# Performance work log

Hardware: AMD Instinct MI355X
Metric: run time of the kernel (lower is better)

## Reference

```python
import jax, jax.numpy as jnp
import numpy as np

B, T, C = 2, 2048, 1024
N_HEAD = 16
HEAD_DIM = C // N_HEAD

def setup_inputs() -> dict:
    key = jax.random.key(0)
    k1, k2, k3 = jax.random.split(key, 3)
    x = jax.random.normal(k1, (B, T, C), dtype=jnp.float32)
    # Dense kernel init scale ~ 1/sqrt(fan_in) for stable softmax
    w_attn = jax.random.normal(k2, (C, 3 * C), dtype=jnp.float32) / np.sqrt(C)
    w_proj = jax.random.normal(k3, (C, C), dtype=jnp.float32) / np.sqrt(C)
    return {"x": x, "w_attn": w_attn, "w_proj": w_proj}

def reference(x, w_attn, w_proj):
    Bc, Tc, Cc = x.shape
    # QKV projection (use_bias=False)
    qkv = x @ w_attn  # [B, T, 3C]
    q, k, v = jnp.split(qkv, 3, axis=-1)
    # [B, T, C] -> [B, H, T, D]
    def heads(a):
        return a.reshape(Bc, Tc, N_HEAD, HEAD_DIM).swapaxes(1, 2)
    q, k, v = heads(q), heads(k), heads(v)
    scale = 1.0 / jnp.sqrt(jnp.asarray(HEAD_DIM, dtype=x.dtype))
    attn = jnp.einsum('bhqd,bhkd->bhqk', q, k) * scale  # [B, H, T, T]
    attn = jax.nn.softmax(attn, axis=-1)
    # dropout=0.0 / deterministic -> identity
    y = jnp.einsum('bhqk,bhkd->bhqd', attn, v)  # [B, H, T, D]
    y = y.swapaxes(1, 2).reshape(Bc, Tc, Cc)
    return y @ w_proj  # output projection, no bias, dropout identity
```

## Files before the change

### kernel.cpp

```cpp
#include <hip/hip_runtime.h>
#include <hip/hip_bf16.h>

#define B_   2
#define T_   2048
#define C_   1024
#define NH_  16
#define HD_  64

typedef __attribute__((ext_vector_type(8))) short short8;
typedef __attribute__((ext_vector_type(4))) float float4_;
typedef __attribute__((ext_vector_type(4))) _Float16 half4_;
typedef __attribute__((ext_vector_type(2))) __fp16  fp16x2;
typedef __attribute__((ext_vector_type(4))) unsigned short ushort4_;

static __device__ __forceinline__ unsigned short f2bf(float f) {
    union { float f; unsigned u; } v; v.f = f;
    unsigned r = v.u + 0x7fffu + ((v.u >> 16) & 1u);
    return (unsigned short)(r >> 16);
}

static __device__ __forceinline__ void g2l16(const void* g, void* l) {
    __builtin_amdgcn_global_load_lds(
        (const __attribute__((address_space(1))) void*)g,
        (__attribute__((address_space(3))) void*)l, 16, 0, 0);
}

__global__ __launch_bounds__(256) void prep(
    const float* __restrict__ x,      unsigned short* __restrict__ xb,
    const float* __restrict__ wA,     unsigned short* __restrict__ wTa,
    const float* __restrict__ wP,     unsigned short* __restrict__ wTp)
{
    const int t = threadIdx.x;
    int blk = blockIdx.x;
    if (blk < 2048) {
        int i = blk * 256 + t;
        const float4* p = (const float4*)x + (size_t)i * 2;
        float4 a = p[0], b = p[1];
        short8 o;
        o[0]=f2bf(a.x); o[1]=f2bf(a.y); o[2]=f2bf(a.z); o[3]=f2bf(a.w);
        o[4]=f2bf(b.x); o[5]=f2bf(b.y); o[6]=f2bf(b.z); o[7]=f2bf(b.w);
        *((short8*)xb + i) = o;
        return;
    }
    blk -= 2048;
    const float* in; unsigned short* out; int Cc;
    if (blk < 16 * 48) { in = wA; out = wTa; Cc = 3072; }
    else               { blk -= 16 * 48; in = wP; out = wTp; Cc = 1024; }
    const int r0 = (blk % 16) * 64, c0 = (blk / 16) * 64;
    const int R = 1024;
    __shared__ __align__(16) unsigned short Ts[64][72];
    #pragma unroll
    for (int cc = 0; cc < 2; ++cc) {
        int c = cc * 256 + t;
        int r = c >> 3, col = (c & 7) * 8;
        const float* p = in + (size_t)(r0 + r) * Cc + c0 + col;
        #pragma unroll
        for (int i = 0; i < 8; ++i) Ts[col + i][r] = f2bf(p[i]);
    }
    __syncthreads();
    #pragma unroll
    for (int cc = 0; cc < 2; ++cc) {
        int c = cc * 256 + t;
        int cr = c >> 3, oc = (c & 7) * 8;
        uint4 v = *(const uint4*)(&Ts[cr][oc]);
        *(uint4*)(out + (size_t)(c0 + cr) * R + r0 + oc) = v;
    }
}

template <bool C_F32, int BM, bool WRITE_VT>
__global__ __launch_bounds__(256) void gemm_bt(
    const unsigned short* __restrict__ A,
    const unsigned short* __restrict__ Bt,
    void* __restrict__ Cv, unsigned short* __restrict__ vt,
    int M, int N, int K)
{
    __shared__ __align__(16) unsigned short As[BM * 32];
    __shared__ __align__(16) unsigned short Bs[128 * 32];
    const int t = threadIdx.x, lane = t & 63, w = t >> 6;
    const int quad = lane >> 4, ln = lane & 15;
    const int bm = blockIdx.x, bn = blockIdx.y;
    constexpr int NI = (BM == 128) ? 4 : 2;
    const int mw = (BM == 128) ? (w & 1) * 64 : 0;
    const int nw = (BM == 128) ? (w >> 1) * 64 : w * 32;
    float4_ acc[4][NI] = {};

    constexpr int AROWS = BM / 4;
    const unsigned short* Ag = A  + (size_t)(bm * BM + w * AROWS + (lane >> 2)) * K + (lane & 3) * 8;
    const unsigned short* Bg = Bt + (size_t)(bn * 128 + w * 32 + (lane >> 2)) * K + (lane & 3) * 8;
    unsigned short* lA = &As[(w * AROWS) * 32 + lane * 8];
    unsigned short* lB = &Bs[(w * 32) * 32 + lane * 8];

    for (int k0 = 0; k0 < K; k0 += 32) {
        g2l16(Ag + k0, lA);
        if (BM == 128) g2l16(Ag + (size_t)16 * K + k0, lA + 16 * 32);
        g2l16(Bg + k0,                  lB);
        g2l16(Bg + (size_t)16 * K + k0, lB + 16 * 32);
        __syncthreads();
        short8 a[4], b[NI];
        #pragma unroll
        for (int i = 0; i < 4; ++i)
            a[i] = *(const short8*)(&As[(mw + i * 16 + ln) * 32 + quad * 8]);
        #pragma unroll
        for (int i = 0; i < NI; ++i)
            b[i] = *(const short8*)(&Bs[(nw + i * 16 + ln) * 32 + quad * 8]);
        #pragma unroll
        for (int mi = 0; mi < 4; ++mi)
            #pragma unroll
            for (int ni = 0; ni < NI; ++ni)
                acc[mi][ni] = __builtin_amdgcn_mfma_f32_16x16x32_bf16(
                    a[mi], b[ni], acc[mi][ni], 0, 0, 0);
        __syncthreads();
    }

    const int row0 = bm * BM + mw + quad * 4;
    const int col0 = bn * 128 + nw + ln;
    #pragma unroll
    for (int mi = 0; mi < 4; ++mi)
        #pragma unroll
        for (int ni = 0; ni < NI; ++ni) {
            #pragma unroll
            for (int i = 0; i < 4; ++i) {
                size_t idx = (size_t)(row0 + mi * 16 + i) * N + col0 + ni * 16;
                if (C_F32) ((float*)Cv)[idx] = acc[mi][ni][i];
                else       ((unsigned short*)Cv)[idx] = f2bf(acc[mi][ni][i]);
            }
            if (WRITE_VT && col0 + ni * 16 >= 2 * C_) {
                int d     = col0 + ni * 16 - 2 * C_;
                int token = row0 + mi * 16;
                int b     = token >> 11, tloc = token & 2047;
                union { fp16x2 h2[2]; ushort4_ u4; } pk;
                pk.h2[0] = __builtin_amdgcn_cvt_pkrtz(acc[mi][ni][0], acc[mi][ni][1]);
                pk.h2[1] = __builtin_amdgcn_cvt_pkrtz(acc[mi][ni][2], acc[mi][ni][3]);
                *(ushort4_*)(vt + ((size_t)b * 1024 + d) * T_ + tloc) = pk.u4;
            }
        }
}

__device__ __forceinline__ void attn_tile(
    const unsigned short (*Ksb)[72], const unsigned short (*Vsb)[72],
    const short8 (&qf)[2][2], float4_ (&ot)[4][2], float (&ls)[2],
    int quad, int ln)
{
    const float C1 = 0.125f * 1.44269504f;
    const float C2 = 8.0f * 1.44269504f;
    half4_ pf[4][2];
    #pragma unroll
    for (int ct = 0; ct < 4; ++ct) {
        short8 kb0 = *(const short8*)(&Ksb[ct * 16 + ln][quad * 8]);
        short8 kb1 = *(const short8*)(&Ksb[ct * 16 + ln][32 + quad * 8]);
        #pragma unroll
        for (int qm = 0; qm < 2; ++qm) {
            float4_ st = {};
            st = __builtin_amdgcn_mfma_f32_16x16x32_bf16(kb0, qf[qm][0], st, 0, 0, 0);
            st = __builtin_amdgcn_mfma_f32_16x16x32_bf16(kb1, qf[qm][1], st, 0, 0, 0);
            float p0 = __builtin_amdgcn_exp2f(st[0] * C1 - C2);
            float p1 = __builtin_amdgcn_exp2f(st[1] * C1 - C2);
            float p2 = __builtin_amdgcn_exp2f(st[2] * C1 - C2);
            float p3 = __builtin_amdgcn_exp2f(st[3] * C1 - C2);
            ls[qm] += (p0 + p1) + (p2 + p3);
            union { fp16x2 h2[2]; half4_ h4; } u;
            u.h2[0] = __builtin_amdgcn_cvt_pkrtz(p0, p1);
            u.h2[1] = __builtin_amdgcn_cvt_pkrtz(p2, p3);
            pf[ct][qm] = u.h4;
        }
    }
    const char* vbase = (const char*)(&Vsb[0][0]);
    const int rsw = ln & 8;
    #pragma unroll
    for (int dt = 0; dt < 4; ++dt) {
        int roff = (dt * 16 + ln) * 144;
        #pragma unroll
        for (int ct = 0; ct < 4; ++ct) {
            half4_ va = *(const half4_*)(vbase + roff + ((ct * 32 + quad * 8) ^ rsw));
            #pragma unroll
            for (int qm = 0; qm < 2; ++qm)
                ot[dt][qm] = __builtin_amdgcn_mfma_f32_16x16x16f16(
                    va, pf[ct][qm], ot[dt][qm], 0, 0, 0);
        }
    }
}

__global__ __launch_bounds__(256) void attn(
    const unsigned short* __restrict__ qkv,
    const unsigned short* __restrict__ vt,
    unsigned short* __restrict__ Y)
{
    __shared__ __align__(16) unsigned short Qs[128][72];
    __shared__ __align__(16) unsigned short Ks[2][64][72];
    __shared__ __align__(16) unsigned short Vs[2][64][72];

    const int t = threadIdx.x;
    const int qt = blockIdx.x, bh = blockIdx.y;
    const int b = bh >> 4, h = bh & 15;
    const int lane = t & 63, w = t >> 6;
    const int quad = lane >> 4, ln = lane & 15;

    const unsigned short* Qg  = qkv + (size_t)b * T_ * (3 * C_) + (size_t)h * HD_;
    const unsigned short* Kg  = Qg + C_;
    const unsigned short* Vtg = vt + (size_t)bh * HD_ * T_;

    #pragma unroll
    for (int cc = 0; cc < 4; ++cc) {
        int c = cc * 256 + t;
        int r = c >> 3, col = (c & 7) * 8;
        *(uint4*)(&Qs[r][col]) = *(const uint4*)(Qg + (size_t)(qt * 128 + r) * (3 * C_) + col);
    }

    const int r0 = t >> 3, c0v = (t & 7) * 8;
    const int r1 = r0 + 32;
    const int vsw = r0 & 8;

    auto load_kv = [&](uint4& k0, uint4& k1, uint4& v0, uint4& v1, int kb) {
        k0 = *(const uint4*)(Kg + (size_t)(kb + r0) * (3 * C_) + c0v);
        k1 = *(const uint4*)(Kg + (size_t)(kb + r1) * (3 * C_) + c0v);
        v0 = *(const uint4*)(Vtg + (size_t)r0 * T_ + kb + c0v);
        v1 = *(const uint4*)(Vtg + (size_t)r1 * T_ + kb + c0v);
    };
    auto store_kv = [&](unsigned short (*Kb)[72], unsigned short (*Vb)[72],
                        uint4 k0, uint4 k1, uint4 v0, uint4 v1) {
        *(uint4*)(&Kb[r0][c0v]) = k0;
        *(uint4*)(&Kb[r1][c0v]) = k1;
        if (vsw) {
            uint4 s;
            s.x = v0.z; s.y = v0.w; s.z = v0.x; s.w = v0.y; v0 = s;
            s.x = v1.z; s.y = v1.w; s.z = v1.x; s.w = v1.y; v1 = s;
        }
        *(uint4*)(&Vb[r0][c0v]) = v0;
        *(uint4*)(&Vb[r1][c0v]) = v1;
    };

    uint4 ka0, ka1, va0, va1, kb0r, kb1r, vb0r, vb1r;
    load_kv(ka0, ka1, va0, va1, 0);

    __syncthreads();

    short8 qf[2][2];
    #pragma unroll
    for (int qm = 0; qm < 2; ++qm)
        #pragma unroll
        for (int dh = 0; dh < 2; ++dh)
            qf[qm][dh] = *(const short8*)(&Qs[w * 32 + qm * 16 + ln][dh * 32 + quad * 8]);

    store_kv(Ks[0], Vs[0], ka0, ka1, va0, va1);
    load_kv(kb0r, kb1r, vb0r, vb1r, 64);
    __syncthreads();

    float4_ ot[4][2] = {};
    float ls[2] = {0.f, 0.f};

    constexpr int NT = T_ / 64;
    for (int it = 0; it < NT; it += 2) {
        if (it + 1 < NT) store_kv(Ks[1], Vs[1], kb0r, kb1r, vb0r, vb1r);
        if (it + 2 < NT) load_kv(ka0, ka1, va0, va1, (it + 2) * 64);
        attn_tile(Ks[0], Vs[0], qf, ot, ls, quad, ln);
        __syncthreads();

        if (it + 2 < NT) store_kv(Ks[0], Vs[0], ka0, ka1, va0, va1);
        if (it + 3 < NT) load_kv(kb0r, kb1r, vb0r, vb1r, (it + 3) * 64);
        if (it + 1 < NT) attn_tile(Ks[1], Vs[1], qf, ot, ls, quad, ln);
        __syncthreads();
    }

    #pragma unroll
    for (int qm = 0; qm < 2; ++qm) {
        ls[qm] += __shfl_xor(ls[qm], 16, 64);
        ls[qm] += __shfl_xor(ls[qm], 32, 64);
    }

    #pragma unroll
    for (int qm = 0; qm < 2; ++qm) {
        unsigned short* Yr = Y + ((size_t)b * T_ + qt * 128 + w * 32 + qm * 16 + ln) * C_ + h * HD_;
        float inv = 1.0f / ls[qm];
        #pragma unroll
        for (int dt = 0; dt < 4; ++dt)
            #pragma unroll
            for (int i = 0; i < 4; ++i)
                Yr[dt * 16 + quad * 4 + i] = f2bf(ot[dt][qm][i] * inv);
    }
}

extern "C" void kernel_launch(void* const* d_in, const int* in_sizes, int n_in,
                              void* d_out, int out_size, void* d_ws, size_t ws_size,
                              hipStream_t stream)
{
    const float* x      = (const float*)d_in[0];
    const float* w_attn = (const float*)d_in[1];
    const float* w_proj = (const float*)d_in[2];
    float* out = (float*)d_out;

    unsigned short* qkv = (unsigned short*)d_ws;
    unsigned short* y   = qkv + (size_t)4096 * 3072;
    unsigned short* wTa = y   + (size_t)4096 * 1024;
    unsigned short* wTp = wTa + (size_t)3072 * 1024;
    unsigned short* vt  = wTp + (size_t)1024 * 1024;
    unsigned short* xb  = y;

    prep<<<2048 + 16 * 48 + 16 * 16, 256, 0, stream>>>(x, xb, w_attn, wTa, w_proj, wTp);

    gemm_bt<false, 128, true><<<dim3(32, 24), 256, 0, stream>>>(
        xb, wTa, qkv, vt, 4096, 3072, 1024);
    attn<<<dim3(16, 32), 256, 0, stream>>>(qkv, vt, y);
    gemm_bt<true, 64, false><<<dim3(64, 8), 256, 0, stream>>>(
        y, wTp, out, nullptr, 4096, 1024, 1024);
}
```

Before: 190.0 us.

## Halve attention query tile to 64 rows with 128-thread blocks and aliased LDS

The attention kernel now processes 64 query rows per block with 2 waves instead of 128 rows with 4 waves, doubling the grid to 1024 blocks. The Q staging buffer is aliased onto the second K/V buffer, which cuts LDS per block to 36 KB so more blocks can be resident per CU. The goal is better occupancy and load balance across CUs. In exchange, each K/V tile loaded into LDS is reused by fewer query rows, so global and LDS traffic per unit of work doubles.

```diff
diff --git a/kernel.cpp b/kernel.cpp
--- a/kernel.cpp
+++ b/kernel.cpp
@@ -180,14 +180,17 @@
     }
 }
 
-__global__ __launch_bounds__(256) void attn(
+__global__ __launch_bounds__(128) void attn(
     const unsigned short* __restrict__ qkv,
     const unsigned short* __restrict__ vt,
     unsigned short* __restrict__ Y)
 {
-    __shared__ __align__(16) unsigned short Qs[128][72];
-    __shared__ __align__(16) unsigned short Ks[2][64][72];
-    __shared__ __align__(16) unsigned short Vs[2][64][72];
+    __shared__ __align__(16) char smem_[36864];
+    auto Ks0 = (unsigned short (*)[72])(smem_);
+    auto Vs0 = (unsigned short (*)[72])(smem_ + 9216);
+    auto Ks1 = (unsigned short (*)[72])(smem_ + 18432);
+    auto Vs1 = (unsigned short (*)[72])(smem_ + 27648);
+    auto Qs  = (unsigned short (*)[72])(smem_ + 18432);
 
     const int t = threadIdx.x;
     const int qt = blockIdx.x, bh = blockIdx.y;
@@ -201,36 +204,36 @@
 
     #pragma unroll
     for (int cc = 0; cc < 4; ++cc) {
-        int c = cc * 256 + t;
+        int c = cc * 128 + t;
         int r = c >> 3, col = (c & 7) * 8;
-        *(uint4*)(&Qs[r][col]) = *(const uint4*)(Qg + (size_t)(qt * 128 + r) * (3 * C_) + col);
-    }
-
-    const int r0 = t >> 3, c0v = (t & 7) * 8;
-    const int r1 = r0 + 32;
-    const int vsw = r0 & 8;
-
-    auto load_kv = [&](uint4& k0, uint4& k1, uint4& v0, uint4& v1, int kb) {
-        k0 = *(const uint4*)(Kg + (size_t)(kb + r0) * (3 * C_) + c0v);
-        k1 = *(const uint4*)(Kg + (size_t)(kb + r1) * (3 * C_) + c0v);
-        v0 = *(const uint4*)(Vtg + (size_t)r0 * T_ + kb + c0v);
-        v1 = *(const uint4*)(Vtg + (size_t)r1 * T_ + kb + c0v);
+        *(uint4*)(&Qs[r][col]) = *(const uint4*)(Qg + (size_t)(qt * 64 + r) * (3 * C_) + col);
+    }
+
+    const int rr = t >> 3, c0v = (t & 7) * 8;
+    const int vsw = rr & 8;
+
+    auto load_kv = [&](uint4 (&k)[4], uint4 (&v)[4], int kb) {
+        #pragma unroll
+        for (int cc = 0; cc < 4; ++cc) {
+            int r = cc * 16 + rr;
+            k[cc] = *(const uint4*)(Kg + (size_t)(kb + r) * (3 * C_) + c0v);
+            v[cc] = *(const uint4*)(Vtg + (size_t)r * T_ + kb + c0v);
+        }
     };
     auto store_kv = [&](unsigned short (*Kb)[72], unsigned short (*Vb)[72],
-                        uint4 k0, uint4 k1, uint4 v0, uint4 v1) {
-        *(uint4*)(&Kb[r0][c0v]) = k0;
-        *(uint4*)(&Kb[r1][c0v]) = k1;
-        if (vsw) {
-            uint4 s;
-            s.x = v0.z; s.y = v0.w; s.z = v0.x; s.w = v0.y; v0 = s;
-            s.x = v1.z; s.y = v1.w; s.z = v1.x; s.w = v1.y; v1 = s;
-        }
-        *(uint4*)(&Vb[r0][c0v]) = v0;
-        *(uint4*)(&Vb[r1][c0v]) = v1;
+                        uint4 (&k)[4], uint4 (&v)[4]) {
+        #pragma unroll
+        for (int cc = 0; cc < 4; ++cc) {
+            int r = cc * 16 + rr;
+            *(uint4*)(&Kb[r][c0v]) = k[cc];
+            uint4 vv = v[cc];
+            if (vsw) { uint4 s; s.x = vv.z; s.y = vv.w; s.z = vv.x; s.w = vv.y; vv = s; }
+            *(uint4*)(&Vb[r][c0v]) = vv;
+        }
     };
 
-    uint4 ka0, ka1, va0, va1, kb0r, kb1r, vb0r, vb1r;
-    load_kv(ka0, ka1, va0, va1, 0);
+    uint4 ka[4], va[4], kb_[4], vb_[4];
+    load_kv(ka, va, 0);
 
     __syncthreads();
 
@@ -241,8 +244,8 @@
         for (int dh = 0; dh < 2; ++dh)
             qf[qm][dh] = *(const short8*)(&Qs[w * 32 + qm * 16 + ln][dh * 32 + quad * 8]);
 
-    store_kv(Ks[0], Vs[0], ka0, ka1, va0, va1);
-    load_kv(kb0r, kb1r, vb0r, vb1r, 64);
+    store_kv(Ks0, Vs0, ka, va);
+    load_kv(kb_, vb_, 64);
     __syncthreads();
 
     float4_ ot[4][2] = {};
@@ -250,14 +253,14 @@
 
     constexpr int NT = T_ / 64;
     for (int it = 0; it < NT; it += 2) {
-        if (it + 1 < NT) store_kv(Ks[1], Vs[1], kb0r, kb1r, vb0r, vb1r);
-        if (it + 2 < NT) load_kv(ka0, ka1, va0, va1, (it + 2) * 64);
-        attn_tile(Ks[0], Vs[0], qf, ot, ls, quad, ln);
+        if (it + 1 < NT) store_kv(Ks1, Vs1, kb_, vb_);
+        if (it + 2 < NT) load_kv(ka, va, (it + 2) * 64);
+        attn_tile(Ks0, Vs0, qf, ot, ls, quad, ln);
         __syncthreads();
 
-        if (it + 2 < NT) store_kv(Ks[0], Vs[0], ka0, ka1, va0, va1);
-        if (it + 3 < NT) load_kv(kb0r, kb1r, vb0r, vb1r, (it + 3) * 64);
-        if (it + 1 < NT) attn_tile(Ks[1], Vs[1], qf, ot, ls, quad, ln);
+        if (it + 2 < NT) store_kv(Ks0, Vs0, ka, va);
+        if (it + 3 < NT) load_kv(kb_, vb_, (it + 3) * 64);
+        if (it + 1 < NT) attn_tile(Ks1, Vs1, qf, ot, ls, quad, ln);
         __syncthreads();
     }
 
@@ -269,7 +272,7 @@
 
     #pragma unroll
     for (int qm = 0; qm < 2; ++qm) {
-        unsigned short* Yr = Y + ((size_t)b * T_ + qt * 128 + w * 32 + qm * 16 + ln) * C_ + h * HD_;
+        unsigned short* Yr = Y + ((size_t)b * T_ + qt * 64 + w * 32 + qm * 16 + ln) * C_ + h * HD_;
         float inv = 1.0f / ls[qm];
         #pragma unroll
         for (int dt = 0; dt < 4; ++dt)
@@ -299,7 +302,7 @@
 
     gemm_bt<false, 128, true><<<dim3(32, 24), 256, 0, stream>>>(
         xb, wTa, qkv, vt, 4096, 3072, 1024);
-    attn<<<dim3(16, 32), 256, 0, stream>>>(qkv, vt, y);
+    attn<<<dim3(32, 32), 128, 0, stream>>>(qkv, vt, y);
     gemm_bt<true, 64, false><<<dim3(64, 8), 256, 0, stream>>>(
         y, wTp, out, nullptr, 4096, 1024, 1024);
 }
```

Measured after the change: 234.5 us. +23.4%, slower.

## Double-buffer GEMM LDS tiles and skip redundant V row-major stores

Applied to the files above, without the earlier changes.

Splits the GEMM shared-memory tiles into two buffers so the next K-slice's global-to-LDS loads are issued before computing on the current slice, overlapping memory latency with MFMA work. Also, for QKV blocks covering the V columns, it writes only the transposed fp16 V output and no longer writes the row-major copy, cutting global stores. The cost is doubled LDS use per block, which may lower occupancy, and it relies on later kernels not reading V from the row-major buffer.

```diff
diff --git a/kernel.cpp b/kernel.cpp
--- a/kernel.cpp
+++ b/kernel.cpp
@@ -74,8 +74,8 @@
     void* __restrict__ Cv, unsigned short* __restrict__ vt,
     int M, int N, int K)
 {
-    __shared__ __align__(16) unsigned short As[BM * 32];
-    __shared__ __align__(16) unsigned short Bs[128 * 32];
+    __shared__ __align__(16) unsigned short As[2][BM * 32];
+    __shared__ __align__(16) unsigned short Bs[2][128 * 32];
     const int t = threadIdx.x, lane = t & 63, w = t >> 6;
     const int quad = lane >> 4, ln = lane & 15;
     const int bm = blockIdx.x, bn = blockIdx.y;
@@ -87,22 +87,30 @@
     constexpr int AROWS = BM / 4;
     const unsigned short* Ag = A  + (size_t)(bm * BM + w * AROWS + (lane >> 2)) * K + (lane & 3) * 8;
     const unsigned short* Bg = Bt + (size_t)(bn * 128 + w * 32 + (lane >> 2)) * K + (lane & 3) * 8;
-    unsigned short* lA = &As[(w * AROWS) * 32 + lane * 8];
-    unsigned short* lB = &Bs[(w * 32) * 32 + lane * 8];
-
-    for (int k0 = 0; k0 < K; k0 += 32) {
-        g2l16(Ag + k0, lA);
-        if (BM == 128) g2l16(Ag + (size_t)16 * K + k0, lA + 16 * 32);
-        g2l16(Bg + k0,                  lB);
-        g2l16(Bg + (size_t)16 * K + k0, lB + 16 * 32);
-        __syncthreads();
+    const int lAo = (w * AROWS) * 32 + lane * 8;
+    const int lBo = (w * 32) * 32 + lane * 8;
+
+    auto stage = [&](int buf, int k0) {
+        g2l16(Ag + k0, &As[buf][lAo]);
+        if (BM == 128) g2l16(Ag + (size_t)16 * K + k0, &As[buf][lAo + 16 * 32]);
+        g2l16(Bg + k0,                  &Bs[buf][lBo]);
+        g2l16(Bg + (size_t)16 * K + k0, &Bs[buf][lBo + 16 * 32]);
+    };
+
+    stage(0, 0);
+    __syncthreads();
+
+    const int NTK = K / 32;
+    for (int tk = 0; tk < NTK; ++tk) {
+        const int cur = tk & 1;
+        if (tk + 1 < NTK) stage(cur ^ 1, (tk + 1) * 32);
         short8 a[4], b[NI];
         #pragma unroll
         for (int i = 0; i < 4; ++i)
-            a[i] = *(const short8*)(&As[(mw + i * 16 + ln) * 32 + quad * 8]);
+            a[i] = *(const short8*)(&As[cur][(mw + i * 16 + ln) * 32 + quad * 8]);
         #pragma unroll
         for (int i = 0; i < NI; ++i)
-            b[i] = *(const short8*)(&Bs[(nw + i * 16 + ln) * 32 + quad * 8]);
+            b[i] = *(const short8*)(&Bs[cur][(nw + i * 16 + ln) * 32 + quad * 8]);
         #pragma unroll
         for (int mi = 0; mi < 4; ++mi)
             #pragma unroll
@@ -114,17 +122,20 @@
 
     const int row0 = bm * BM + mw + quad * 4;
     const int col0 = bn * 128 + nw + ln;
+    const bool vblk = WRITE_VT && (bn >= 16);
     #pragma unroll
     for (int mi = 0; mi < 4; ++mi)
         #pragma unroll
         for (int ni = 0; ni < NI; ++ni) {
-            #pragma unroll
-            for (int i = 0; i < 4; ++i) {
-                size_t idx = (size_t)(row0 + mi * 16 + i) * N + col0 + ni * 16;
-                if (C_F32) ((float*)Cv)[idx] = acc[mi][ni][i];
-                else       ((unsigned short*)Cv)[idx] = f2bf(acc[mi][ni][i]);
+            if (!vblk) {
+                #pragma unroll
+                for (int i = 0; i < 4; ++i) {
+                    size_t idx = (size_t)(row0 + mi * 16 + i) * N + col0 + ni * 16;
+                    if (C_F32) ((float*)Cv)[idx] = acc[mi][ni][i];
+                    else       ((unsigned short*)Cv)[idx] = f2bf(acc[mi][ni][i]);
+                }
             }
-            if (WRITE_VT && col0 + ni * 16 >= 2 * C_) {
+            if (vblk) {
                 int d     = col0 + ni * 16 - 2 * C_;
                 int token = row0 + mi * 16;
                 int b     = token >> 11, tloc = token & 2047;
```

New measurement: 182.4 us. 4.0% less time.
